# Kernel tuning notes

Measured on AMD Instinct MI355X. Metric: run time of the kernel, lower is better.

Reference implementation:

```python
import jax, jax.numpy as jnp
import numpy as np

IN_DIM = 4096
OUT_DIM = 4096
BLOCK = 256
RANK = 16
B_IN = IN_DIM // BLOCK   # 16
B_OUT = OUT_DIM // BLOCK # 16


def setup_inputs() -> dict:
    key = jax.random.key(0)
    k1, k2, k3, k4, k5 = jax.random.split(key, 5)
    x = jax.random.normal(k1, (2, 1024, IN_DIM), dtype=jnp.float32)
    # S ~ U[0, 2)
    S = jax.random.uniform(k2, (B_OUT, B_IN, RANK), dtype=jnp.float32, minval=0.0, maxval=2.0)
    std = np.sqrt(0.02).astype(np.float32)
    U = jax.random.normal(k3, (B_OUT, RANK, BLOCK), dtype=jnp.float32) * std
    Vt = jax.random.normal(k4, (B_IN, BLOCK, RANK), dtype=jnp.float32) * std
    # kaiming_uniform_ on a (1, out_dim) tensor with default a=sqrt(5): bound = 1/sqrt(fan_in) = 1/sqrt(out_dim)
    bound = float(1.0 / np.sqrt(OUT_DIM))
    bias = jax.random.uniform(k5, (OUT_DIM,), dtype=jnp.float32, minval=-bound, maxval=bound)
    return {"x": x, "S": S, "U": U, "Vt": Vt, "bias": bias}


def reference(x, S, U, Vt, bias):
    # Faithful to Blast.forward: it reconstructs the dense weight by running
    # forward2 on an identity matrix (which ALSO adds bias to every row of W),
    # then computes addmm(bias, x, W).
    # Block (i_in, i_out) of W0 = Vt[i_in] @ diag(S[i_out, i_in]) @ U[i_out].
    W0 = jnp.einsum('ipr,oir,orq->ipoq', Vt, S, U).reshape(IN_DIM, OUT_DIM)
    W = W0 + bias[None, :]  # identity-trick: forward2(I) adds bias to each of the in_dim rows
    out = x @ W + bias      # [B, S, out_dim]
    return out
```

## Files before the change

kernel.cpp:

```cpp
#include <hip/hip_runtime.h>

#define IN_DIM  4096
#define OUT_DIM 4096
#define RANK    16
#define NBLK    16
#define KDIM    256

typedef __attribute__((ext_vector_type(8))) __bf16 bf16x8;
typedef __attribute__((ext_vector_type(4))) __bf16 bf16x4;
typedef __attribute__((ext_vector_type(4))) float  f32x4;


__device__ __forceinline__ void split_bf16(float v, __bf16& h, __bf16& l) {
    h = (__bf16)v;
    l = (__bf16)(v - (float)h);
}

__global__ __launch_bounds__(256) void build_packs(const float* __restrict__ S,
                                                   const float* __restrict__ U,
                                                   const float* __restrict__ Vt,
                                                   bf16x8* __restrict__ Bhi,
                                                   bf16x8* __restrict__ Vhi,
                                                   bf16x8* __restrict__ Vlo) {
    const int blk = blockIdx.x;
    if (blk < 512) {
        int t  = blk * 256 + threadIdx.x;
        int c  = t & 15;
        int ko = (t >> 4) & 31;
        int nt = t >> 9;
        int o  = nt >> 4;
        int i  = ko >> 1;
        int q  = ((nt & 15) << 4) | c;
        int r0 = (ko & 1) << 3;
        const float* Sp = S + ((o * NBLK + i) * RANK + r0);
        const float* Up = U + (size_t)o * RANK * 256 + q;
        bf16x8 hi;
#pragma unroll
        for (int j = 0; j < 8; ++j) {
            float w = Sp[j] * Up[(size_t)(r0 + j) * 256];
            hi[j] = (__bf16)w;
        }
        Bhi[t] = hi;
    } else {
        int t  = (blk - 512) * 256 + threadIdx.x;
        int c  = t & 15;
        int p0 = (t >> 4) << 3;
        int i  = t >> 9;
        int pbase = (p0 & 255);
        const float* vp = Vt + ((size_t)(i * 256 + pbase)) * RANK + c;
        bf16x8 hi, lo;
#pragma unroll
        for (int j = 0; j < 8; ++j) {
            float w = vp[(size_t)j * RANK];
            __bf16 h, l;
            split_bf16(w, h, l);
            hi[j] = h; lo[j] = l;
        }
        Vhi[t] = hi;
        Vlo[t] = lo;
    }
}

__global__ __launch_bounds__(256) void factor_mfma(const float* __restrict__ x,
                                                   const bf16x8* __restrict__ Vhi,
                                                   const bf16x8* __restrict__ Vlo,
                                                   bf16x4* __restrict__ Ahi4,
                                                   bf16x4* __restrict__ Alo4,
                                                   float* __restrict__ rowsum_p,
                                                   int M) {
    const int tid = threadIdx.x;
    const int l   = tid & 63;
    const int w   = tid >> 6;
    const int job = blockIdx.x * 4 + w;
    const int i   = job & 15;
    const int mt  = job >> 4;
    const int row = l & 15;
    const int qt  = l >> 4;

    const float* xp = x + (size_t)(mt * 16 + row) * IN_DIM + i * 256 + qt * 8;

    f32x4 acc = {0.f, 0.f, 0.f, 0.f};
    float rs = 0.f;
#pragma unroll
    for (int ks = 0; ks < 8; ++ks) {
        float4 a = *reinterpret_cast<const float4*>(xp + ks * 32);
        float4 b = *reinterpret_cast<const float4*>(xp + ks * 32 + 4);
        rs += (a.x + a.y) + (a.z + a.w) + (b.x + b.y) + (b.z + b.w);
        float vv[8] = {a.x, a.y, a.z, a.w, b.x, b.y, b.z, b.w};
        bf16x8 xh, xl;
#pragma unroll
        for (int jj = 0; jj < 8; ++jj) {
            __bf16 h, lo_;
            split_bf16(vv[jj], h, lo_);
            xh[jj] = h; xl[jj] = lo_;
        }
        size_t vidx = (size_t)((i * 8 + ks) * 4 + qt) * 16 + row;
        bf16x8 vh = Vhi[vidx];
        bf16x8 vl = Vlo[vidx];
        acc = __builtin_amdgcn_mfma_f32_16x16x32_bf16(vh, xh, acc, 0, 0, 0);
        acc = __builtin_amdgcn_mfma_f32_16x16x32_bf16(vh, xl, acc, 0, 0, 0);
        acc = __builtin_amdgcn_mfma_f32_16x16x32_bf16(vl, xh, acc, 0, 0, 0);
    }

    rs += __shfl_xor(rs, 16, 64);
    rs += __shfl_xor(rs, 32, 64);
    if (l < 16)
        rowsum_p[(size_t)i * M + mt * 16 + l] = rs;

    bf16x4 hi, lo;
#pragma unroll
    for (int reg = 0; reg < 4; ++reg) {
        __bf16 h, lo_;
        split_bf16(acc[reg], h, lo_);
        hi[reg] = h; lo[reg] = lo_;
    }
    size_t o4 = ((size_t)(mt * 32 + i * 2 + (l >> 5)) * 16 + row) * 2 + ((l >> 4) & 1);
    Ahi4[o4] = hi;
    Alo4[o4] = lo;
}

__global__ __launch_bounds__(256, 3) void apply_mfma(const bf16x8* __restrict__ Ahi,
                                                     const bf16x8* __restrict__ Alo,
                                                     const bf16x8* __restrict__ Bhi,
                                                     const float* __restrict__ rowsum_p,
                                                     const float* __restrict__ bias,
                                                     float* __restrict__ out, int M) {
    __shared__ bf16x8 smem[2][1536];
    __shared__ float rstot_s[128];

    const int nb  = blockIdx.x;
    const int q   = gridDim.x >> 3;
    const int lg  = (nb & 7) * q + (nb >> 3);
    const int mr  = lg & 15;
    const int nc  = lg >> 4;
    const int m0  = mr * 128, n0 = nc * 128;
    const int mtb0 = m0 >> 4;
    const int ntb0 = n0 >> 4;

    const int tid = threadIdx.x;
    const int l   = tid & 63;
    const int w   = __builtin_amdgcn_readfirstlane(tid >> 6);
    const int wm  = w & 1, wn = w >> 1;
    const int kq  = l >> 4, c = l & 15;

#define STAGE(s_, buf_)                                                              \
    {                                                                                \
        _Pragma("unroll")                                                            \
        for (int j = 0; j < 6; ++j) {                                                \
            const int sl = w * 6 + j;                                                \
            const bf16x8* gbase;                                                     \
            if (sl < 8)                                                              \
                gbase = Ahi + ((size_t)((mtb0 + sl) * 32 + 4 * (s_)) * 16);          \
            else if (sl < 16)                                                        \
                gbase = Alo + ((size_t)((mtb0 + sl - 8) * 32 + 4 * (s_)) * 16);      \
            else                                                                     \
                gbase = Bhi + ((size_t)((ntb0 + sl - 16) * 32 + 4 * (s_)) * 16);     \
            __builtin_amdgcn_global_load_lds(                                        \
                (const __attribute__((address_space(1))) unsigned*)(gbase + l),      \
                (__attribute__((address_space(3))) unsigned*)&smem[buf_][sl * 64],   \
                16, 0, 0);                                                           \
        }                                                                            \
    }

    f32x4 acc[4][4];
#pragma unroll
    for (int f = 0; f < 4; ++f)
#pragma unroll
        for (int nf = 0; nf < 4; ++nf) acc[f][nf] = f32x4{0.f, 0.f, 0.f, 0.f};

    STAGE(0, 0);
    if (tid < 128) {
        float ssum = 1.0f;
#pragma unroll
        for (int i = 0; i < NBLK; ++i) ssum += rowsum_p[(size_t)i * M + m0 + tid];
        rstot_s[tid] = ssum;
    }
    __syncthreads();

    for (int s = 0; s < 8; ++s) {
        if (s < 7) STAGE(s + 1, (s + 1) & 1);
        const bf16x8* sb = smem[s & 1];
        bf16x8 ah[4], al[4];
#pragma unroll
        for (int f = 0; f < 4; ++f) {
            ah[f] = sb[(wm * 4 + f) * 64 + l];
            al[f] = sb[512 + (wm * 4 + f) * 64 + l];
        }
#pragma unroll
        for (int nf = 0; nf < 4; ++nf) {
            bf16x8 bh = sb[1024 + (wn * 4 + nf) * 64 + l];
#pragma unroll
            for (int f = 0; f < 4; ++f) {
                acc[f][nf] = __builtin_amdgcn_mfma_f32_16x16x32_bf16(ah[f], bh, acc[f][nf], 0, 0, 0);
                acc[f][nf] = __builtin_amdgcn_mfma_f32_16x16x32_bf16(al[f], bh, acc[f][nf], 0, 0, 0);
            }
        }
        __syncthreads();
    }
#undef STAGE

#pragma unroll
    for (int f = 0; f < 4; ++f) {
        const int rloc = wm * 64 + f * 16 + kq * 4;
        const int rowb = m0 + rloc;
        float rsv[4];
#pragma unroll
        for (int reg = 0; reg < 4; ++reg) rsv[reg] = rstot_s[rloc + reg];
#pragma unroll
        for (int nf = 0; nf < 4; ++nf) {
            const int n = n0 + wn * 64 + nf * 16 + c;
            const float bv = bias[n];
#pragma unroll
            for (int reg = 0; reg < 4; ++reg)
                out[(size_t)(rowb + reg) * OUT_DIM + n] = acc[f][nf][reg] + rsv[reg] * bv;
        }
    }
}

extern "C" void kernel_launch(void* const* d_in, const int* in_sizes, int n_in,
                              void* d_out, int out_size, void* d_ws, size_t ws_size,
                              hipStream_t stream) {
    const float* x    = (const float*)d_in[0];
    const float* S    = (const float*)d_in[1];
    const float* U    = (const float*)d_in[2];
    const float* Vt   = (const float*)d_in[3];
    const float* bias = (const float*)d_in[4];
    float* out = (float*)d_out;
    const int M = in_sizes[0] / IN_DIM;

    char* ws = (char*)d_ws;
    bf16x8* Bhi     = (bf16x8*)ws;
    bf16x8* Ahi     = (bf16x8*)(ws + (2u << 20));
    bf16x8* Alo     = (bf16x8*)(ws + (3u << 20));
    bf16x8* Vhi     = (bf16x8*)(ws + (4u << 20));
    bf16x8* Vlo     = (bf16x8*)(ws + (4u << 20) + (128u << 10));
    float* rowsum_p = (float*)(ws + (4u << 20) + (256u << 10));

    build_packs<<<544, 256, 0, stream>>>(S, U, Vt, Bhi, Vhi, Vlo);
    factor_mfma<<<M / 4, 256, 0, stream>>>(x, Vhi, Vlo,
                                           (bf16x4*)Ahi, (bf16x4*)Alo, rowsum_p, M);
    apply_mfma<<<(M / 128) * (OUT_DIM / 128), 256, 0, stream>>>(
        Ahi, Alo, Bhi, rowsum_p, bias, out, M);
}
```

Baseline: 108.9 us.

## Enlarge apply_mfma tile to 128x256 with 512 threads and deeper K stages

The apply kernel now uses 512-thread blocks covering a 128x256 output tile, so each block loads its A hi/lo fragments once for twice as many output columns. Each stage also covers twice the K depth, halving the number of loop iterations and barriers. The LDS buffer grows to 2x4096 bf16x8, which together with the larger block lowers the number of resident blocks per CU. The grid halves, which may leave some compute units idle.

```diff
diff --git a/kernel.cpp b/kernel.cpp
--- a/kernel.cpp
+++ b/kernel.cpp
@@ -119,13 +119,13 @@
     Alo4[o4] = lo;
 }
 
-__global__ __launch_bounds__(256, 3) void apply_mfma(const bf16x8* __restrict__ Ahi,
+__global__ __launch_bounds__(512, 2) void apply_mfma(const bf16x8* __restrict__ Ahi,
                                                      const bf16x8* __restrict__ Alo,
                                                      const bf16x8* __restrict__ Bhi,
                                                      const float* __restrict__ rowsum_p,
                                                      const float* __restrict__ bias,
                                                      float* __restrict__ out, int M) {
-    __shared__ bf16x8 smem[2][1536];
+    __shared__ bf16x8 smem[2][4096];
     __shared__ float rstot_s[128];
 
     const int nb  = blockIdx.x;
@@ -133,7 +133,7 @@
     const int lg  = (nb & 7) * q + (nb >> 3);
     const int mr  = lg & 15;
     const int nc  = lg >> 4;
-    const int m0  = mr * 128, n0 = nc * 128;
+    const int m0  = mr * 128, n0 = nc * 256;
     const int mtb0 = m0 >> 4;
     const int ntb0 = n0 >> 4;
 
@@ -146,18 +146,28 @@
 #define STAGE(s_, buf_)                                                              \
     {                                                                                \
         _Pragma("unroll")                                                            \
-        for (int j = 0; j < 6; ++j) {                                                \
-            const int sl = w * 6 + j;                                                \
+        for (int j = 0; j < 8; ++j) {                                                \
+            const int u = w * 8 + j;                                                 \
             const bf16x8* gbase;                                                     \
-            if (sl < 8)                                                              \
-                gbase = Ahi + ((size_t)((mtb0 + sl) * 32 + 4 * (s_)) * 16);          \
-            else if (sl < 16)                                                        \
-                gbase = Alo + ((size_t)((mtb0 + sl - 8) * 32 + 4 * (s_)) * 16);      \
-            else                                                                     \
-                gbase = Bhi + ((size_t)((ntb0 + sl - 16) * 32 + 4 * (s_)) * 16);     \
+            unsigned loff;                                                           \
+            if (u < 16) {                                                            \
+                gbase = Ahi + ((size_t)((mtb0 + (u >> 1)) * 32 + 8 * (s_)            \
+                                        + (u & 1) * 4) * 16);                        \
+                loff  = (unsigned)(((u >> 1) * 8 + (u & 1) * 4) * 16);               \
+            } else if (u < 32) {                                                     \
+                const int v = u - 16;                                                \
+                gbase = Alo + ((size_t)((mtb0 + (v >> 1)) * 32 + 8 * (s_)            \
+                                        + (v & 1) * 4) * 16);                        \
+                loff  = 1024u + (unsigned)(((v >> 1) * 8 + (v & 1) * 4) * 16);       \
+            } else {                                                                 \
+                const int v = u - 32;                                                \
+                gbase = Bhi + ((size_t)((ntb0 + (v >> 1)) * 32 + 8 * (s_)            \
+                                        + (v & 1) * 4) * 16);                        \
+                loff  = 2048u + (unsigned)(((v >> 1) * 8 + (v & 1) * 4) * 16);       \
+            }                                                                        \
             __builtin_amdgcn_global_load_lds(                                        \
                 (const __attribute__((address_space(1))) unsigned*)(gbase + l),      \
-                (__attribute__((address_space(3))) unsigned*)&smem[buf_][sl * 64],   \
+                (__attribute__((address_space(3))) unsigned*)&smem[buf_][loff],      \
                 16, 0, 0);                                                           \
         }                                                                            \
     }
@@ -177,22 +187,27 @@
     }
     __syncthreads();
 
-    for (int s = 0; s < 8; ++s) {
-        if (s < 7) STAGE(s + 1, (s + 1) & 1);
+    for (int s = 0; s < 4; ++s) {
+        if (s < 3) STAGE(s + 1, (s + 1) & 1);
         const bf16x8* sb = smem[s & 1];
-        bf16x8 ah[4], al[4];
-#pragma unroll
-        for (int f = 0; f < 4; ++f) {
-            ah[f] = sb[(wm * 4 + f) * 64 + l];
-            al[f] = sb[512 + (wm * 4 + f) * 64 + l];
-        }
-#pragma unroll
-        for (int nf = 0; nf < 4; ++nf) {
-            bf16x8 bh = sb[1024 + (wn * 4 + nf) * 64 + l];
+#pragma unroll
+        for (int ksl = 0; ksl < 2; ++ksl) {
+            bf16x8 ah[4], al[4];
 #pragma unroll
             for (int f = 0; f < 4; ++f) {
-                acc[f][nf] = __builtin_amdgcn_mfma_f32_16x16x32_bf16(ah[f], bh, acc[f][nf], 0, 0, 0);
-                acc[f][nf] = __builtin_amdgcn_mfma_f32_16x16x32_bf16(al[f], bh, acc[f][nf], 0, 0, 0);
+                const int mt = wm * 4 + f;
+                ah[f] = sb[(mt * 8 + ksl * 4 + kq) * 16 + c];
+                al[f] = sb[1024 + (mt * 8 + ksl * 4 + kq) * 16 + c];
+            }
+#pragma unroll
+            for (int nf = 0; nf < 4; ++nf) {
+                const int nt = wn * 4 + nf;
+                bf16x8 bh = sb[2048 + (nt * 8 + ksl * 4 + kq) * 16 + c];
+#pragma unroll
+                for (int f = 0; f < 4; ++f) {
+                    acc[f][nf] = __builtin_amdgcn_mfma_f32_16x16x32_bf16(ah[f], bh, acc[f][nf], 0, 0, 0);
+                    acc[f][nf] = __builtin_amdgcn_mfma_f32_16x16x32_bf16(al[f], bh, acc[f][nf], 0, 0, 0);
+                }
             }
         }
         __syncthreads();
@@ -239,6 +254,6 @@
     build_packs<<<544, 256, 0, stream>>>(S, U, Vt, Bhi, Vhi, Vlo);
     factor_mfma<<<M / 4, 256, 0, stream>>>(x, Vhi, Vlo,
                                            (bf16x4*)Ahi, (bf16x4*)Alo, rowsum_p, M);
-    apply_mfma<<<(M / 128) * (OUT_DIM / 128), 256, 0, stream>>>(
+    apply_mfma<<<(M / 128) * (OUT_DIM / 256), 512, 0, stream>>>(
         Ahi, Alo, Bhi, rowsum_p, bias, out, M);
 }
```

Result: no change. 109.9 us (+0.9%).

## Fuse Vt packing into factor kernel and merge with B-pack launch

Applied to the files above, without the earlier changes.

Drops the separate Vt hi/lo pack step. The factor stage now reads Vt directly from fp32 memory and splits it into bf16 hi/lo in registers. The factor work and the B-pack work are placed in one kernel launch as disjoint block ranges, removing a launch and a dependency barrier along with the Vhi/Vlo workspace traffic. In exchange, each factor wave does strided scalar loads of Vt and repeats the split conversions redundantly across blocks.

```diff
diff --git a/kernel.cpp b/kernel.cpp
--- a/kernel.cpp
+++ b/kernel.cpp
@@ -16,15 +16,76 @@
     l = (__bf16)(v - (float)h);
 }
 
-__global__ __launch_bounds__(256) void build_packs(const float* __restrict__ S,
-                                                   const float* __restrict__ U,
-                                                   const float* __restrict__ Vt,
-                                                   bf16x8* __restrict__ Bhi,
-                                                   bf16x8* __restrict__ Vhi,
-                                                   bf16x8* __restrict__ Vlo) {
-    const int blk = blockIdx.x;
-    if (blk < 512) {
-        int t  = blk * 256 + threadIdx.x;
+__global__ __launch_bounds__(256) void fused_factor_pack(const float* __restrict__ x,
+                                                         const float* __restrict__ S,
+                                                         const float* __restrict__ U,
+                                                         const float* __restrict__ Vt,
+                                                         bf16x4* __restrict__ Ahi4,
+                                                         bf16x4* __restrict__ Alo4,
+                                                         bf16x8* __restrict__ Bhi,
+                                                         float* __restrict__ rowsum_p,
+                                                         int M) {
+    const int nfac = M >> 2;
+    const int blk  = blockIdx.x;
+    const int tid  = threadIdx.x;
+
+    if (blk < nfac) {
+        const int l   = tid & 63;
+        const int w   = tid >> 6;
+        const int job = blk * 4 + w;
+        const int i   = job & 15;
+        const int mt  = job >> 4;
+        const int row = l & 15;
+        const int qt  = l >> 4;
+
+        const float* xp  = x + (size_t)(mt * 16 + row) * IN_DIM + i * 256 + qt * 8;
+        const float* vtp = Vt + ((size_t)(i * 256 + qt * 8)) * RANK + row;
+
+        f32x4 acc = {0.f, 0.f, 0.f, 0.f};
+        float rs = 0.f;
+#pragma unroll
+        for (int ks = 0; ks < 8; ++ks) {
+            float4 a = *reinterpret_cast<const float4*>(xp + ks * 32);
+            float4 b = *reinterpret_cast<const float4*>(xp + ks * 32 + 4);
+            rs += (a.x + a.y) + (a.z + a.w) + (b.x + b.y) + (b.z + b.w);
+            float vv[8] = {a.x, a.y, a.z, a.w, b.x, b.y, b.z, b.w};
+            bf16x8 xh, xl;
+#pragma unroll
+            for (int jj = 0; jj < 8; ++jj) {
+                __bf16 h, lo_;
+                split_bf16(vv[jj], h, lo_);
+                xh[jj] = h; xl[jj] = lo_;
+            }
+            bf16x8 vh, vl;
+#pragma unroll
+            for (int jj = 0; jj < 8; ++jj) {
+                float v = vtp[(size_t)(ks * 32 + jj) * RANK];
+                __bf16 h, lo_;
+                split_bf16(v, h, lo_);
+                vh[jj] = h; vl[jj] = lo_;
+            }
+            acc = __builtin_amdgcn_mfma_f32_16x16x32_bf16(vh, xh, acc, 0, 0, 0);
+            acc = __builtin_amdgcn_mfma_f32_16x16x32_bf16(vh, xl, acc, 0, 0, 0);
+            acc = __builtin_amdgcn_mfma_f32_16x16x32_bf16(vl, xh, acc, 0, 0, 0);
+        }
+
+        rs += __shfl_xor(rs, 16, 64);
+        rs += __shfl_xor(rs, 32, 64);
+        if (l < 16)
+            rowsum_p[(size_t)i * M + mt * 16 + l] = rs;
+
+        bf16x4 hi, lo;
+#pragma unroll
+        for (int reg = 0; reg < 4; ++reg) {
+            __bf16 h, lo_;
+            split_bf16(acc[reg], h, lo_);
+            hi[reg] = h; lo[reg] = lo_;
+        }
+        size_t o4 = ((size_t)(mt * 32 + i * 2 + (l >> 5)) * 16 + row) * 2 + ((l >> 4) & 1);
+        Ahi4[o4] = hi;
+        Alo4[o4] = lo;
+    } else {
+        int t  = (blk - nfac) * 256 + tid;
         int c  = t & 15;
         int ko = (t >> 4) & 31;
         int nt = t >> 9;
@@ -41,82 +102,7 @@
             hi[j] = (__bf16)w;
         }
         Bhi[t] = hi;
-    } else {
-        int t  = (blk - 512) * 256 + threadIdx.x;
-        int c  = t & 15;
-        int p0 = (t >> 4) << 3;
-        int i  = t >> 9;
-        int pbase = (p0 & 255);
-        const float* vp = Vt + ((size_t)(i * 256 + pbase)) * RANK + c;
-        bf16x8 hi, lo;
-#pragma unroll
-        for (int j = 0; j < 8; ++j) {
-            float w = vp[(size_t)j * RANK];
-            __bf16 h, l;
-            split_bf16(w, h, l);
-            hi[j] = h; lo[j] = l;
-        }
-        Vhi[t] = hi;
-        Vlo[t] = lo;
-    }
-}
-
-__global__ __launch_bounds__(256) void factor_mfma(const float* __restrict__ x,
-                                                   const bf16x8* __restrict__ Vhi,
-                                                   const bf16x8* __restrict__ Vlo,
-                                                   bf16x4* __restrict__ Ahi4,
-                                                   bf16x4* __restrict__ Alo4,
-                                                   float* __restrict__ rowsum_p,
-                                                   int M) {
-    const int tid = threadIdx.x;
-    const int l   = tid & 63;
-    const int w   = tid >> 6;
-    const int job = blockIdx.x * 4 + w;
-    const int i   = job & 15;
-    const int mt  = job >> 4;
-    const int row = l & 15;
-    const int qt  = l >> 4;
-
-    const float* xp = x + (size_t)(mt * 16 + row) * IN_DIM + i * 256 + qt * 8;
-
-    f32x4 acc = {0.f, 0.f, 0.f, 0.f};
-    float rs = 0.f;
-#pragma unroll
-    for (int ks = 0; ks < 8; ++ks) {
-        float4 a = *reinterpret_cast<const float4*>(xp + ks * 32);
-        float4 b = *reinterpret_cast<const float4*>(xp + ks * 32 + 4);
-        rs += (a.x + a.y) + (a.z + a.w) + (b.x + b.y) + (b.z + b.w);
-        float vv[8] = {a.x, a.y, a.z, a.w, b.x, b.y, b.z, b.w};
-        bf16x8 xh, xl;
-#pragma unroll
-        for (int jj = 0; jj < 8; ++jj) {
-            __bf16 h, lo_;
-            split_bf16(vv[jj], h, lo_);
-            xh[jj] = h; xl[jj] = lo_;
-        }
-        size_t vidx = (size_t)((i * 8 + ks) * 4 + qt) * 16 + row;
-        bf16x8 vh = Vhi[vidx];
-        bf16x8 vl = Vlo[vidx];
-        acc = __builtin_amdgcn_mfma_f32_16x16x32_bf16(vh, xh, acc, 0, 0, 0);
-        acc = __builtin_amdgcn_mfma_f32_16x16x32_bf16(vh, xl, acc, 0, 0, 0);
-        acc = __builtin_amdgcn_mfma_f32_16x16x32_bf16(vl, xh, acc, 0, 0, 0);
-    }
-
-    rs += __shfl_xor(rs, 16, 64);
-    rs += __shfl_xor(rs, 32, 64);
-    if (l < 16)
-        rowsum_p[(size_t)i * M + mt * 16 + l] = rs;
-
-    bf16x4 hi, lo;
-#pragma unroll
-    for (int reg = 0; reg < 4; ++reg) {
-        __bf16 h, lo_;
-        split_bf16(acc[reg], h, lo_);
-        hi[reg] = h; lo[reg] = lo_;
-    }
-    size_t o4 = ((size_t)(mt * 32 + i * 2 + (l >> 5)) * 16 + row) * 2 + ((l >> 4) & 1);
-    Ahi4[o4] = hi;
-    Alo4[o4] = lo;
+    }
 }
 
 __global__ __launch_bounds__(256, 3) void apply_mfma(const bf16x8* __restrict__ Ahi,
@@ -232,13 +218,10 @@
     bf16x8* Bhi     = (bf16x8*)ws;
     bf16x8* Ahi     = (bf16x8*)(ws + (2u << 20));
     bf16x8* Alo     = (bf16x8*)(ws + (3u << 20));
-    bf16x8* Vhi     = (bf16x8*)(ws + (4u << 20));
-    bf16x8* Vlo     = (bf16x8*)(ws + (4u << 20) + (128u << 10));
-    float* rowsum_p = (float*)(ws + (4u << 20) + (256u << 10));
-
-    build_packs<<<544, 256, 0, stream>>>(S, U, Vt, Bhi, Vhi, Vlo);
-    factor_mfma<<<M / 4, 256, 0, stream>>>(x, Vhi, Vlo,
-                                           (bf16x4*)Ahi, (bf16x4*)Alo, rowsum_p, M);
+    float* rowsum_p = (float*)(ws + (4u << 20));
+
+    fused_factor_pack<<<(M / 4) + 512, 256, 0, stream>>>(
+        x, S, U, Vt, (bf16x4*)Ahi, (bf16x4*)Alo, Bhi, rowsum_p, M);
     apply_mfma<<<(M / 128) * (OUT_DIM / 128), 256, 0, stream>>>(
         Ahi, Alo, Bhi, rowsum_p, bias, out, M);
 }
```

Result: faster. 104.4 us (-4.1%).
